# Optimization experiments

Measured on AMD Instinct MI355X. Metric: run time of the kernel, lower is better.

## Reference

```python
import jax, jax.numpy as jnp
import numpy as np

H = 8
DQ = 32
DK = 32
DV = 32
DC = DQ + DK  # concat dim for additive attention


def setup_inputs() -> dict:
    key = jax.random.key(0)
    ks = jax.random.split(key, 8)
    bs, Lq, Lk = 2, 384, 384
    q = jax.random.normal(ks[0], (bs, Lq, H * DQ), jnp.float32)
    k = jax.random.normal(ks[1], (bs, Lk, H * DK), jnp.float32)
    v = jax.random.normal(ks[2], (bs, Lk, H * DV), jnp.float32)
    q_sequence_lengths = jax.random.randint(ks[3], (bs,), 1, Lq + 1, dtype=jnp.int32)
    k_sequence_lengths = jax.random.randint(ks[4], (bs,), 1, Lk + 1, dtype=jnp.int32)
    bound = 1.0 / np.sqrt(DC)
    w1 = jax.random.uniform(ks[5], (H, DC, DC), jnp.float32, -bound, bound)
    b1 = jax.random.uniform(ks[6], (H, DC), jnp.float32, -bound, bound)
    w2 = jax.random.uniform(ks[7], (H, DC), jnp.float32, -1.0, 1.0)
    return {"q": q, "k": k, "v": v,
            "q_sequence_lengths": q_sequence_lengths,
            "k_sequence_lengths": k_sequence_lengths,
            "w1": w1, "b1": b1, "w2": w2}


def reference(q, k, v, q_sequence_lengths, k_sequence_lengths, w1, b1, w2):
    bs, Lq, _ = q.shape
    Lk = k.shape[1]
    # split heads: (b, h, L, d)
    qh = q.reshape(bs, Lq, H, DQ).transpose(0, 2, 1, 3)
    kh = k.reshape(bs, Lk, H, DK).transpose(0, 2, 1, 3)
    vh = v.reshape(bs, Lk, H, DV).transpose(0, 2, 1, 3)
    # additive scores: tanh(cat(q_i, k_j) @ W1 + b1) @ w2
    # cat @ W1 == q @ W1[:DQ] + k @ W1[DQ:]  (avoids materializing the cat)
    qW = jnp.einsum('bhqd,hde->bhqe', qh, w1[:, :DQ, :])
    kW = jnp.einsum('bhkd,hde->bhke', kh, w1[:, DQ:, :])
    hid = jnp.tanh(qW[:, :, :, None, :] + kW[:, :, None, :, :] + b1[None, :, None, None, :])  # (b,h,q,k,DC)
    scores = jnp.einsum('bhqke,he->bhqk', hid, w2)
    # key-side length mask (end padded)
    kmask = jnp.arange(Lk)[None, :] < k_sequence_lengths[:, None]  # (b, Lk)
    scores = jnp.where(kmask[:, None, None, :], scores, jnp.float32(-1e9))
    att = jax.nn.softmax(scores, axis=-1)  # (b,h,q,k)
    out = jnp.einsum('bhqk,bhkd->bqhd', att, vh)  # (b,q,h,DV)
    # query-side length mask zeros out padded query rows
    qmask = jnp.arange(Lq)[None, :] < q_sequence_lengths[:, None]  # (b, Lq)
    out = out * qmask[:, :, None, None].astype(out.dtype)
    return out.reshape(bs, Lq, H * DV), att
```

## Files before the change

kernel.cpp:

```cpp
#include <hip/hip_runtime.h>

#define NH 8
#define LQ 384
#define LK 384
#define BS 2
#define ROWPAD 68

__global__ __launch_bounds__(256) void pre_ek_kernel(
    const float* __restrict__ kin, const float* __restrict__ w1,
    const float* __restrict__ b1, float* __restrict__ ws)
{
    const int bid = blockIdx.x;
    const int bh = bid / 12, kt = bid % 12;
    const int b = bh >> 3, h = bh & 7;
    const int k0 = kt * 32;
    const int lane = threadIdx.x & 63, w = threadIdx.x >> 6;

    float w1c[32];
    const float* w1p = w1 + (size_t)(h * 64 + 32) * 64 + lane;
    #pragma unroll
    for (int d = 0; d < 32; ++d) w1c[d] = w1p[d * 64];
    const float bv = b1[h * 64 + lane];

    #pragma unroll
    for (int s = 0; s < 8; ++s) {
        int kr = w * 8 + s;
        const float* krow = kin + ((size_t)(b * LK + k0 + kr)) * (NH * 32) + h * 32;
        float acc = bv;
        #pragma unroll
        for (int d = 0; d < 32; ++d) acc = __builtin_fmaf(krow[d], w1c[d], acc);
        ws[((size_t)(bh * LK + k0 + kr)) * 64 + lane] = __expf(acc + acc);
    }
}

__global__ __launch_bounds__(256) void attn_kernel(
    const float* __restrict__ qin, const float* __restrict__ vin,
    const int* __restrict__ qlens, const int* __restrict__ klens,
    const float* __restrict__ w1, const float* __restrict__ w2g,
    const float* __restrict__ ws,
    float* __restrict__ outg, float* __restrict__ attg)
{
    __shared__ __align__(16) float buf0[64 * ROWPAD];
    __shared__ __align__(16) float buf1[64 * ROWPAD];
    __shared__ __align__(16) float att_s[8][LK];
    __shared__ __align__(16) float eqs[8 * 64];
    __shared__ __align__(16) float w2s[64];

    const int tid = threadIdx.x, wave = tid >> 6, lane = tid & 63;
    const int bh = blockIdx.x / 48, tile = blockIdx.x % 48;
    const int b = bh >> 3, h = bh & 7;
    const int q0 = tile * 8;
    const int klen = klens[b], qlen = qlens[b];

    const float* ekg = ws + (size_t)bh * LK * 64;

    {
        const float4* w1g = (const float4*)(w1 + (size_t)h * 64 * 64);
        ((float4*)buf1)[tid]       = w1g[tid];
        ((float4*)buf1)[tid + 256] = w1g[tid + 256];
        if (tid < 64) {
            int r = tid >> 3, c = tid & 7;
            ((float4*)att_s)[tid] =
                ((const float4*)(qin + ((size_t)(b * LQ + q0 + r)) * (NH * 32) + h * 32))[c];
        } else if (tid < 80) {
            ((float4*)w2s)[tid - 64] = ((const float4*)(w2g + h * 64))[tid - 64];
        }
    }
    float4 pf[4];
    {
        const float4* src = (const float4*)ekg;
        #pragma unroll
        for (int i = 0; i < 4; ++i) pf[i] = src[tid + 256 * i];
    }
    __syncthreads();

    {
        const float* qa = (const float*)att_s;
        float a0 = 0.f, a1 = 0.f;
        #pragma unroll
        for (int d = 0; d < 32; ++d) {
            float wv = buf1[d * 64 + lane];
            a0 = __builtin_fmaf(qa[wave * 32 + d],       wv, a0);
            a1 = __builtin_fmaf(qa[(wave + 4) * 32 + d], wv, a1);
        }
        eqs[wave * 64 + lane]       = __expf(a0 + a0);
        eqs[(wave + 4) * 64 + lane] = __expf(a1 + a1);
    }
    #pragma unroll
    for (int i = 0; i < 4; ++i) {
        int f = tid + 256 * i;
        ((float4*)(buf0 + (f >> 4) * ROWPAD))[f & 15] = pf[i];
    }
    {
        const float4* src = (const float4*)(ekg + 1 * 64 * 64);
        #pragma unroll
        for (int i = 0; i < 4; ++i) pf[i] = src[tid + 256 * i];
    }
    __syncthreads();

    float sc0[6], sc1[6];
    const float4* eq0p = (const float4*)(eqs + (wave * 2 + 0) * 64);
    const float4* eq1p = (const float4*)(eqs + (wave * 2 + 1) * 64);
    #pragma unroll
    for (int c = 0; c < 6; ++c) {
        if (c < 5) {
            float* bufn = (c & 1) ? buf0 : buf1;
            #pragma unroll
            for (int i = 0; i < 4; ++i) {
                int f = tid + 256 * i;
                ((float4*)(bufn + (f >> 4) * ROWPAD))[f & 15] = pf[i];
            }
        }
        if (c < 4) {
            const float4* src = (const float4*)(ekg + (size_t)(c + 2) * 64 * 64);
            #pragma unroll
            for (int i = 0; i < 4; ++i) pf[i] = src[tid + 256 * i];
        }
        const float* eb = ((c & 1) ? buf1 : buf0) + lane * ROWPAD;
        float s0 = 0.f, s1 = 0.f;
        #pragma unroll
        for (int e4 = 0; e4 < 16; ++e4) {
            float4 kv = *(const float4*)(eb + 4 * e4);
            float4 wv = ((const float4*)w2s)[e4];
            float4 e0 = eq0p[e4];
            float4 e1 = eq1p[e4];
            {
                float t0 = __builtin_fmaf(e0.x, kv.x, 1.f);
                float t1 = __builtin_fmaf(e0.y, kv.y, 1.f);
                float t2 = __builtin_fmaf(e0.z, kv.z, 1.f);
                float t3 = __builtin_fmaf(e0.w, kv.w, 1.f);
                float p12 = t0 * t1, p34 = t2 * t3;
                float n12 = wv.x * t1; n12 = __builtin_fmaf(wv.y, t0, n12);
                float n34 = wv.z * t3; n34 = __builtin_fmaf(wv.w, t2, n34);
                float num = n12 * p34; num = __builtin_fmaf(n34, p12, num);
                s0 = __builtin_fmaf(num, __builtin_amdgcn_rcpf(p12 * p34), s0);
            }
            {
                float t0 = __builtin_fmaf(e1.x, kv.x, 1.f);
                float t1 = __builtin_fmaf(e1.y, kv.y, 1.f);
                float t2 = __builtin_fmaf(e1.z, kv.z, 1.f);
                float t3 = __builtin_fmaf(e1.w, kv.w, 1.f);
                float p12 = t0 * t1, p34 = t2 * t3;
                float n12 = wv.x * t1; n12 = __builtin_fmaf(wv.y, t0, n12);
                float n34 = wv.z * t3; n34 = __builtin_fmaf(wv.w, t2, n34);
                float num = n12 * p34; num = __builtin_fmaf(n34, p12, num);
                s1 = __builtin_fmaf(num, __builtin_amdgcn_rcpf(p12 * p34), s1);
            }
        }
        sc0[c] = s0; sc1[c] = s1;
        if (c < 5) __syncthreads();
    }

    #pragma unroll
    for (int i = 0; i < 2; ++i) {
        const float* scp = i ? sc1 : sc0;
        float s_[6], p[6];
        float m = -3.4e38f;
        #pragma unroll
        for (int j = 0; j < 6; ++j) {
            int kk = j * 64 + lane;
            float v = -2.0f * scp[j];
            s_[j] = (kk < klen) ? v : -3.4e38f;
            m = fmaxf(m, s_[j]);
        }
        #pragma unroll
        for (int off = 32; off >= 1; off >>= 1) m = fmaxf(m, __shfl_xor(m, off));
        float ssum = 0.f;
        #pragma unroll
        for (int j = 0; j < 6; ++j) {
            int kk = j * 64 + lane;
            p[j] = (kk < klen) ? __expf(s_[j] - m) : 0.f;
            ssum += p[j];
        }
        #pragma unroll
        for (int off = 32; off >= 1; off >>= 1) ssum += __shfl_xor(ssum, off);
        float inv = __builtin_amdgcn_rcpf(ssum);
        float* arow = att_s[wave * 2 + i];
        #pragma unroll
        for (int j = 0; j < 6; ++j) arow[j * 64 + lane] = p[j] * inv;
    }

    #pragma unroll
    for (int i3 = 0; i3 < 3; ++i3) {
        int f4i = i3 * 64 + lane;
        int rl = f4i / 96, c4 = f4i % 96;
        float4 av = *(const float4*)(&att_s[wave * 2 + rl][c4 * 4]);
        *(float4*)(attg + ((size_t)(bh * LQ + q0 + wave * 2 + rl)) * LK + c4 * 4) = av;
    }

    const int kf = lane >> 3, dg = lane & 7;
    const float* vrow = vin + (size_t)b * LK * (NH * 32) + h * 32 + kf * (NH * 32) + dg * 4;
    const float* a0p = att_s[wave * 2 + 0];
    const float* a1p = att_s[wave * 2 + 1];
    float oa[2][4] = {{0.f,0.f,0.f,0.f},{0.f,0.f,0.f,0.f}};
    #pragma unroll 8
    for (int k0 = 0; k0 < LK; k0 += 8) {
        float4 vv = *(const float4*)(vrow + (size_t)k0 * (NH * 32));
        float a0 = a0p[k0 + kf];
        float a1 = a1p[k0 + kf];
        oa[0][0] = __builtin_fmaf(a0, vv.x, oa[0][0]);
        oa[0][1] = __builtin_fmaf(a0, vv.y, oa[0][1]);
        oa[0][2] = __builtin_fmaf(a0, vv.z, oa[0][2]);
        oa[0][3] = __builtin_fmaf(a0, vv.w, oa[0][3]);
        oa[1][0] = __builtin_fmaf(a1, vv.x, oa[1][0]);
        oa[1][1] = __builtin_fmaf(a1, vv.y, oa[1][1]);
        oa[1][2] = __builtin_fmaf(a1, vv.z, oa[1][2]);
        oa[1][3] = __builtin_fmaf(a1, vv.w, oa[1][3]);
    }
    #pragma unroll
    for (int i = 0; i < 2; ++i)
        #pragma unroll
        for (int u = 0; u < 4; ++u) {
            float x = oa[i][u];
            x += __shfl_xor(x, 8);
            x += __shfl_xor(x, 16);
            x += __shfl_xor(x, 32);
            oa[i][u] = x;
        }
    if (kf == 0) {
        #pragma unroll
        for (int i = 0; i < 2; ++i) {
            int q = q0 + wave * 2 + i;
            float4 o4;
            o4.x = (q < qlen) ? oa[i][0] : 0.f;
            o4.y = (q < qlen) ? oa[i][1] : 0.f;
            o4.z = (q < qlen) ? oa[i][2] : 0.f;
            o4.w = (q < qlen) ? oa[i][3] : 0.f;
            ((float4*)(outg + ((size_t)(b * LQ + q)) * (NH * 32) + h * 32))[dg] = o4;
        }
    }
}

extern "C" void kernel_launch(void* const* d_in, const int* in_sizes, int n_in,
                              void* d_out, int out_size, void* d_ws, size_t ws_size,
                              hipStream_t stream) {
    const float* q    = (const float*)d_in[0];
    const float* k    = (const float*)d_in[1];
    const float* v    = (const float*)d_in[2];
    const int*   qlen = (const int*)d_in[3];
    const int*   klen = (const int*)d_in[4];
    const float* w1   = (const float*)d_in[5];
    const float* b1   = (const float*)d_in[6];
    const float* w2   = (const float*)d_in[7];
    float* out = (float*)d_out;
    float* att = out + (size_t)BS * LQ * NH * 32;
    float* ws  = (float*)d_ws;

    pre_ek_kernel<<<192, 256, 0, stream>>>(k, w1, b1, ws);
    attn_kernel<<<768, 256, 0, stream>>>(q, v, qlen, klen, w1, w2, ws, out, att);
}
```

Baseline: 115.9 us.

## Transpose precomputed key features to float4-major layout and read directly from global

```diff
diff --git a/kernel.cpp b/kernel.cpp
--- a/kernel.cpp
+++ b/kernel.cpp
@@ -4,12 +4,12 @@
 #define LQ 384
 #define LK 384
 #define BS 2
-#define ROWPAD 68
 
 __global__ __launch_bounds__(256) void pre_ek_kernel(
     const float* __restrict__ kin, const float* __restrict__ w1,
     const float* __restrict__ b1, float* __restrict__ ws)
 {
+    __shared__ float tile[32][65];
     const int bid = blockIdx.x;
     const int bh = bid / 12, kt = bid % 12;
     const int b = bh >> 3, h = bh & 7;
@@ -29,7 +29,19 @@
         float acc = bv;
         #pragma unroll
         for (int d = 0; d < 32; ++d) acc = __builtin_fmaf(krow[d], w1c[d], acc);
-        ws[((size_t)(bh * LK + k0 + kr)) * 64 + lane] = __expf(acc + acc);
+        tile[kr][lane] = __expf(acc + acc);
+    }
+    __syncthreads();
+    #pragma unroll
+    for (int r = 0; r < 2; ++r) {
+        int f = threadIdx.x + r * 256;
+        int e4 = f >> 5, k32 = f & 31;
+        float4 o;
+        o.x = tile[k32][e4 * 4 + 0];
+        o.y = tile[k32][e4 * 4 + 1];
+        o.z = tile[k32][e4 * 4 + 2];
+        o.w = tile[k32][e4 * 4 + 3];
+        ((float4*)ws)[((size_t)(bh * 16 + e4)) * LK + k0 + k32] = o;
     }
 }
 
@@ -40,90 +52,49 @@
     const float* __restrict__ ws,
     float* __restrict__ outg, float* __restrict__ attg)
 {
-    __shared__ __align__(16) float buf0[64 * ROWPAD];
-    __shared__ __align__(16) float buf1[64 * ROWPAD];
     __shared__ __align__(16) float att_s[8][LK];
     __shared__ __align__(16) float eqs[8 * 64];
-    __shared__ __align__(16) float w2s[64];
+    __shared__ __align__(16) float w2s[4][64];
 
     const int tid = threadIdx.x, wave = tid >> 6, lane = tid & 63;
     const int bh = blockIdx.x / 48, tile = blockIdx.x % 48;
     const int b = bh >> 3, h = bh & 7;
     const int q0 = tile * 8;
     const int klen = klens[b], qlen = qlens[b];
-
-    const float* ekg = ws + (size_t)bh * LK * 64;
+    const int r0 = wave * 2;
 
     {
-        const float4* w1g = (const float4*)(w1 + (size_t)h * 64 * 64);
-        ((float4*)buf1)[tid]       = w1g[tid];
-        ((float4*)buf1)[tid + 256] = w1g[tid + 256];
-        if (tid < 64) {
-            int r = tid >> 3, c = tid & 7;
-            ((float4*)att_s)[tid] =
-                ((const float4*)(qin + ((size_t)(b * LQ + q0 + r)) * (NH * 32) + h * 32))[c];
-        } else if (tid < 80) {
-            ((float4*)w2s)[tid - 64] = ((const float4*)(w2g + h * 64))[tid - 64];
-        }
-    }
-    float4 pf[4];
-    {
-        const float4* src = (const float4*)ekg;
-        #pragma unroll
-        for (int i = 0; i < 4; ++i) pf[i] = src[tid + 256 * i];
-    }
-    __syncthreads();
-
-    {
-        const float* qa = (const float*)att_s;
+        const float* w1p = w1 + (size_t)h * 64 * 64 + lane;
+        const float* q0p = qin + ((size_t)(b * LQ + q0 + r0)) * (NH * 32) + h * 32;
+        const float* q1p = q0p + (NH * 32);
         float a0 = 0.f, a1 = 0.f;
         #pragma unroll
         for (int d = 0; d < 32; ++d) {
-            float wv = buf1[d * 64 + lane];
-            a0 = __builtin_fmaf(qa[wave * 32 + d],       wv, a0);
-            a1 = __builtin_fmaf(qa[(wave + 4) * 32 + d], wv, a1);
-        }
-        eqs[wave * 64 + lane]       = __expf(a0 + a0);
-        eqs[(wave + 4) * 64 + lane] = __expf(a1 + a1);
-    }
-    #pragma unroll
-    for (int i = 0; i < 4; ++i) {
-        int f = tid + 256 * i;
-        ((float4*)(buf0 + (f >> 4) * ROWPAD))[f & 15] = pf[i];
-    }
-    {
-        const float4* src = (const float4*)(ekg + 1 * 64 * 64);
-        #pragma unroll
-        for (int i = 0; i < 4; ++i) pf[i] = src[tid + 256 * i];
-    }
-    __syncthreads();
-
-    float sc0[6], sc1[6];
-    const float4* eq0p = (const float4*)(eqs + (wave * 2 + 0) * 64);
-    const float4* eq1p = (const float4*)(eqs + (wave * 2 + 1) * 64);
-    #pragma unroll
-    for (int c = 0; c < 6; ++c) {
-        if (c < 5) {
-            float* bufn = (c & 1) ? buf0 : buf1;
-            #pragma unroll
-            for (int i = 0; i < 4; ++i) {
-                int f = tid + 256 * i;
-                ((float4*)(bufn + (f >> 4) * ROWPAD))[f & 15] = pf[i];
-            }
-        }
-        if (c < 4) {
-            const float4* src = (const float4*)(ekg + (size_t)(c + 2) * 64 * 64);
-            #pragma unroll
-            for (int i = 0; i < 4; ++i) pf[i] = src[tid + 256 * i];
-        }
-        const float* eb = ((c & 1) ? buf1 : buf0) + lane * ROWPAD;
-        float s0 = 0.f, s1 = 0.f;
-        #pragma unroll
-        for (int e4 = 0; e4 < 16; ++e4) {
-            float4 kv = *(const float4*)(eb + 4 * e4);
-            float4 wv = ((const float4*)w2s)[e4];
-            float4 e0 = eq0p[e4];
-            float4 e1 = eq1p[e4];
+            float wv = w1p[d * 64];
+            a0 = __builtin_fmaf(q0p[d], wv, a0);
+            a1 = __builtin_fmaf(q1p[d], wv, a1);
+        }
+        eqs[(r0 + 0) * 64 + lane] = __expf(a0 + a0);
+        eqs[(r0 + 1) * 64 + lane] = __expf(a1 + a1);
+        w2s[wave][lane] = w2g[h * 64 + lane];
+    }
+
+    float sc0[6] = {0.f,0.f,0.f,0.f,0.f,0.f};
+    float sc1[6] = {0.f,0.f,0.f,0.f,0.f,0.f};
+    const float4* ekq  = (const float4*)ws + ((size_t)bh * 16) * LK + lane;
+    const float4* eq0p = (const float4*)(eqs + (r0 + 0) * 64);
+    const float4* eq1p = (const float4*)(eqs + (r0 + 1) * 64);
+    const float4* w2p  = (const float4*)(&w2s[wave][0]);
+
+    #pragma unroll 4
+    for (int e4 = 0; e4 < 16; ++e4) {
+        float4 e0 = eq0p[e4];
+        float4 e1 = eq1p[e4];
+        float4 wv = w2p[e4];
+        const float4* kp = ekq + e4 * LK;
+        #pragma unroll
+        for (int c = 0; c < 6; ++c) {
+            float4 kv = kp[c * 64];
             {
                 float t0 = __builtin_fmaf(e0.x, kv.x, 1.f);
                 float t1 = __builtin_fmaf(e0.y, kv.y, 1.f);
@@ -133,7 +104,7 @@
                 float n12 = wv.x * t1; n12 = __builtin_fmaf(wv.y, t0, n12);
                 float n34 = wv.z * t3; n34 = __builtin_fmaf(wv.w, t2, n34);
                 float num = n12 * p34; num = __builtin_fmaf(n34, p12, num);
-                s0 = __builtin_fmaf(num, __builtin_amdgcn_rcpf(p12 * p34), s0);
+                sc0[c] = __builtin_fmaf(num, __builtin_amdgcn_rcpf(p12 * p34), sc0[c]);
             }
             {
                 float t0 = __builtin_fmaf(e1.x, kv.x, 1.f);
@@ -144,16 +115,15 @@
                 float n12 = wv.x * t1; n12 = __builtin_fmaf(wv.y, t0, n12);
                 float n34 = wv.z * t3; n34 = __builtin_fmaf(wv.w, t2, n34);
                 float num = n12 * p34; num = __builtin_fmaf(n34, p12, num);
-                s1 = __builtin_fmaf(num, __builtin_amdgcn_rcpf(p12 * p34), s1);
+                sc1[c] = __builtin_fmaf(num, __builtin_amdgcn_rcpf(p12 * p34), sc1[c]);
             }
         }
-        sc0[c] = s0; sc1[c] = s1;
-        if (c < 5) __syncthreads();
     }
 
     #pragma unroll
     for (int i = 0; i < 2; ++i) {
         const float* scp = i ? sc1 : sc0;
+        int q = q0 + r0 + i;
         float s_[6], p[6];
         float m = -3.4e38f;
         #pragma unroll
@@ -175,23 +145,20 @@
         #pragma unroll
         for (int off = 32; off >= 1; off >>= 1) ssum += __shfl_xor(ssum, off);
         float inv = __builtin_amdgcn_rcpf(ssum);
-        float* arow = att_s[wave * 2 + i];
-        #pragma unroll
-        for (int j = 0; j < 6; ++j) arow[j * 64 + lane] = p[j] * inv;
-    }
-
-    #pragma unroll
-    for (int i3 = 0; i3 < 3; ++i3) {
-        int f4i = i3 * 64 + lane;
-        int rl = f4i / 96, c4 = f4i % 96;
-        float4 av = *(const float4*)(&att_s[wave * 2 + rl][c4 * 4]);
-        *(float4*)(attg + ((size_t)(bh * LQ + q0 + wave * 2 + rl)) * LK + c4 * 4) = av;
+        float* arow = att_s[r0 + i];
+        float* ag = attg + ((size_t)(bh * LQ + q)) * LK;
+        #pragma unroll
+        for (int j = 0; j < 6; ++j) {
+            float a = p[j] * inv;
+            arow[j * 64 + lane] = a;
+            ag[j * 64 + lane]   = a;
+        }
     }
 
     const int kf = lane >> 3, dg = lane & 7;
     const float* vrow = vin + (size_t)b * LK * (NH * 32) + h * 32 + kf * (NH * 32) + dg * 4;
-    const float* a0p = att_s[wave * 2 + 0];
-    const float* a1p = att_s[wave * 2 + 1];
+    const float* a0p = att_s[r0 + 0];
+    const float* a1p = att_s[r0 + 1];
     float oa[2][4] = {{0.f,0.f,0.f,0.f},{0.f,0.f,0.f,0.f}};
     #pragma unroll 8
     for (int k0 = 0; k0 < LK; k0 += 8) {
@@ -220,7 +187,7 @@
     if (kf == 0) {
         #pragma unroll
         for (int i = 0; i < 2; ++i) {
-            int q = q0 + wave * 2 + i;
+            int q = q0 + r0 + i;
             float4 o4;
             o4.x = (q < qlen) ? oa[i][0] : 0.f;
             o4.y = (q < qlen) ? oa[i][1] : 0.f;
```

Result: faster. 105.1 us (-9.3%).
